# Kernel tuning notes

Measured on AMD Instinct MI355X. Metric: run time of the kernel, lower is better.

The kernel has to match this reference:

```python
import jax, jax.numpy as jnp
import numpy as np

B, S, N_IN, N_OUT = 4, 192, 256, 1

def setup_inputs() -> dict:
    key = jax.random.key(0)
    ks = jax.random.split(key, 7)
    scale = 1.0 / np.sqrt(N_IN)
    return {
        "h_head": jax.random.normal(ks[0], (B, S, N_IN), jnp.float32),
        "h_dep": jax.random.normal(ks[1], (B, S, N_IN), jnp.float32),
        "h_sib": jax.random.normal(ks[2], (B, S, N_IN), jnp.float32),
        "W_tri": jax.random.normal(ks[3], (N_OUT, N_IN, N_IN, N_IN), jnp.float32) * (scale / N_IN),
        "U_hd": jax.random.normal(ks[4], (N_OUT, N_IN, N_IN), jnp.float32) * scale,
        "V_hs": jax.random.normal(ks[5], (N_OUT, N_IN, N_IN), jnp.float32) * scale,
        "Z_ds": jax.random.normal(ks[6], (N_OUT, N_IN, N_IN), jnp.float32) * scale,
        "bias": jnp.zeros((N_OUT,), jnp.float32),
    }

def reference(h_head, h_dep, h_sib, W_tri, U_hd, V_hs, Z_ds, bias):
    # biaffine terms: [b, x, y, o]
    s_hd = jnp.einsum('bhi,oij,bdj->bhdo', h_head, U_hd, h_dep)
    s_hs = jnp.einsum('bhi,oij,bsj->bhso', h_head, V_hs, h_sib)
    s_ds = jnp.einsum('bdi,oij,bsj->bdso', h_dep, Z_ds, h_sib)
    # trilinear term: note j,k of W_tri appear nowhere else, so they are
    # reduced first (w_red[o,i] = sum_{j,k} W_tri[o,i,j,k]) — same math as
    # torch.einsum('bhi,bdi,bsi,oijk->bhdso', ...).
    w_red = jnp.sum(W_tri, axis=(2, 3))  # [o, i]
    s_tri = jnp.einsum('bhi,bdi,bsi,oi->bhdso', h_head, h_dep, h_sib, w_red)
    scores = (s_tri
              + s_hd[:, :, :, None, :]   # unsqueeze sib axis
              + s_hs[:, :, None, :, :]   # unsqueeze dep axis
              + s_ds[:, None, :, :, :]   # unsqueeze head axis
              + bias)
    return scores[..., 0]  # n_out == 1 -> squeeze last dim
```

## Files before the change

kernel.cpp:

```cpp
#include <hip/hip_runtime.h>
#include <stdint.h>

#define NB 4
#define SS 192
#define NI 256

typedef __attribute__((ext_vector_type(8))) short bf16x8;
typedef __attribute__((ext_vector_type(16))) float f32x16;

__device__ __forceinline__ uint16_t f2bf(float f) {
  union { float f; uint32_t u; } v; v.f = f;
  return (uint16_t)((v.u + 0x7FFFu + ((v.u >> 16) & 1u)) >> 16);
}

__device__ __forceinline__ uint4 pack8(const float4 a, const float4 b) {
  uint4 r;
  r.x = (uint32_t)f2bf(a.x) | ((uint32_t)f2bf(a.y) << 16);
  r.y = (uint32_t)f2bf(a.z) | ((uint32_t)f2bf(a.w) << 16);
  r.z = (uint32_t)f2bf(b.x) | ((uint32_t)f2bf(b.y) << 16);
  r.w = (uint32_t)f2bf(b.z) | ((uint32_t)f2bf(b.w) << 16);
  return r;
}

__device__ __forceinline__ uint32_t bfmul2(uint32_t x, uint32_t y) {
  union { float f; uint32_t u; } xa, xb, ya, yb, r0, r1;
  xa.u = x << 16;        ya.u = y << 16;
  xb.u = x & 0xFFFF0000u; yb.u = y & 0xFFFF0000u;
  r0.f = xa.f * ya.f;
  r1.f = xb.f * yb.f;
  uint32_t lo = (r0.u + 0x7FFFu + ((r0.u >> 16) & 1u)) >> 16;
  uint32_t hi = (r1.u + 0x7FFFu + ((r1.u >> 16) & 1u)) >> 16;
  return lo | (hi << 16);
}


__global__ __launch_bounds__(256) void k0(
    const float* __restrict__ W,
    const float* __restrict__ h_head, const float* __restrict__ h_dep, const float* __restrict__ h_sib,
    const float* __restrict__ U, const float* __restrict__ V, const float* __restrict__ Z,
    float* __restrict__ partial,
    uint16_t* __restrict__ HH, uint16_t* __restrict__ HD, uint16_t* __restrict__ HS,
    uint16_t* __restrict__ U16, uint16_t* __restrict__ V16, uint16_t* __restrict__ Z16) {
  __shared__ float red[4];
  const int bi = blockIdx.x, tid = threadIdx.x;
  if (bi < 2048) {
    const float4* pw = (const float4*)(W + (size_t)bi * 8192);
    float4 a = {0.f, 0.f, 0.f, 0.f};
    #pragma unroll
    for (int it = 0; it < 8; ++it) {
      const float4 v = pw[it * 256 + tid];
      a.x += v.x; a.y += v.y; a.z += v.z; a.w += v.w;
    }
    float s = (a.x + a.y) + (a.z + a.w);
    for (int off = 32; off > 0; off >>= 1) s += __shfl_down(s, off, 64);
    if ((tid & 63) == 0) red[tid >> 6] = s;
    __syncthreads();
    if (tid == 0) partial[bi] = red[0] + red[1] + red[2] + red[3];
    return;
  }
  const int rl = tid >> 5, c8 = tid & 31;
  if (bi < 2144) {
    const int g = (bi - 2048) * 8 + rl;
    const int dst = g * 32 + (c8 ^ (g & 15));
    const int srci = g * 64 + c8 * 2;
    { const float4 x = ((const float4*)h_head)[srci], y = ((const float4*)h_head)[srci + 1];
      ((uint4*)HH)[dst] = pack8(x, y); }
    { const float4 x = ((const float4*)h_dep)[srci], y = ((const float4*)h_dep)[srci + 1];
      ((uint4*)HD)[dst] = pack8(x, y); }
    { const float4 x = ((const float4*)h_sib)[srci], y = ((const float4*)h_sib)[srci + 1];
      ((uint4*)HS)[dst] = pack8(x, y); }
  } else {
    const int g = (bi - 2144) * 8 + rl;
    const int dst = g * 32 + (c8 ^ (g & 15));
    const int srci = g * 64 + c8 * 2;
    { const float4 x = ((const float4*)U)[srci], y = ((const float4*)U)[srci + 1];
      ((uint4*)U16)[dst] = pack8(x, y); }
    { const float4 x = ((const float4*)V)[srci], y = ((const float4*)V)[srci + 1];
      ((uint4*)V16)[dst] = pack8(x, y); }
    { const float4 x = ((const float4*)Z)[srci], y = ((const float4*)Z)[srci + 1];
      ((uint4*)Z16)[dst] = pack8(x, y); }
  }
}

__global__ __launch_bounds__(256, 2) void k_s1(
    const uint16_t* __restrict__ HD, const uint16_t* __restrict__ HS,
    const uint16_t* __restrict__ U16, const uint16_t* __restrict__ V16, const uint16_t* __restrict__ Z16,
    uint16_t* __restrict__ dU16, uint16_t* __restrict__ T216, uint16_t* __restrict__ TZ16) {
  __shared__ __align__(16) uint16_t Ah[192 * 128];
  __shared__ __align__(16) uint16_t Bh[128 * 128];
  const int which = blockIdx.x, nt = blockIdx.y, b = blockIdx.z;
  const uint16_t* As = (which == 0) ? HD : HS;
  const uint16_t* Bs = (which == 0) ? U16 : (which == 1) ? V16 : Z16;
  uint16_t* Os = (which == 0) ? dU16 : (which == 1) ? T216 : TZ16;
  const int tid = threadIdx.x, lane = tid & 63, w = tid >> 6;
  const int l31 = lane & 31, l5 = lane >> 5;
  const int N0 = nt * 128;
  f32x16 acc[6] = {};

  #pragma unroll
  for (int kh = 0; kh < 2; ++kh) {
    const int kbase = kh * 128;
    if (kh) __syncthreads();
    #pragma unroll
    for (int i = 0; i < 12; ++i) {
      const int slot = i * 256 + tid;
      const int row = slot >> 4, ck = slot & 15;
      const uint16_t* src = As + (size_t)(b * SS + row) * NI + kbase + ck * 8;
      __builtin_amdgcn_global_load_lds((const __attribute__((address_space(1))) void*)src,
          (__attribute__((address_space(3))) void*)(Ah + (size_t)slot * 8), 16, 0, 0);
    }
    #pragma unroll
    for (int i = 0; i < 8; ++i) {
      const int slot = i * 256 + tid;
      const int row = slot >> 4, ck = slot & 15;
      const uint16_t* src = Bs + (size_t)(N0 + row) * NI + kbase + ck * 8;
      __builtin_amdgcn_global_load_lds((const __attribute__((address_space(1))) void*)src,
          (__attribute__((address_space(3))) void*)(Bh + (size_t)slot * 8), 16, 0, 0);
    }
    __syncthreads();
    const int brow = w * 32 + l31;
    const int bbyte = brow * 256;
    const int bmask = brow & 15;
    #pragma unroll
    for (int ks = 0; ks < 8; ++ks) {
      const int sl = ks * 2 + l5;
      bf16x8 bf = *reinterpret_cast<const bf16x8*>((const char*)Bh + bbyte + ((sl ^ bmask) << 4));
      #pragma unroll
      for (int mt = 0; mt < 6; ++mt) {
        const int ar = mt * 32 + l31;
        bf16x8 af = *reinterpret_cast<const bf16x8*>((const char*)Ah + ar * 256 + ((sl ^ (ar & 15)) << 4));
        acc[mt] = __builtin_amdgcn_mfma_f32_32x32x16_bf16(af, bf, acc[mt], 0, 0, 0);
      }
    }
  }
  const int n = N0 + w * 32 + l31;
  const int nck = n >> 3, npos = n & 7;
  #pragma unroll
  for (int mt = 0; mt < 6; ++mt) {
    #pragma unroll
    for (int r = 0; r < 16; ++r) {
      const int m = mt * 32 + (r & 3) + 8 * (r >> 2) + 4 * l5;
      Os[(size_t)(b * SS + m) * NI + ((nck ^ (m & 15)) << 3) + npos] = f2bf(acc[mt][r]);
    }
  }
}

__global__ __launch_bounds__(384, 1) void k_s2(
    const uint16_t* __restrict__ HH, const uint16_t* __restrict__ HD,
    const uint16_t* __restrict__ dU16, const uint16_t* __restrict__ T216, const uint16_t* __restrict__ TZ16,
    float* __restrict__ s_hd, float* __restrict__ s_hs, float* __restrict__ s_ds) {
  __shared__ __align__(16) uint16_t Ah[192 * 128];
  __shared__ __align__(16) uint16_t Bh[192 * 128];
  const int which = blockIdx.x, b = blockIdx.y;
  const uint16_t* As = (which == 2) ? HD : HH;
  const uint16_t* Bs = (which == 0) ? dU16 : (which == 1) ? T216 : TZ16;
  float* Os = (which == 0) ? s_hd : (which == 1) ? s_hs : s_ds;
  const int tid = threadIdx.x, lane = tid & 63, w = tid >> 6;
  const int l31 = lane & 31, l5 = lane >> 5;
  f32x16 acc[6] = {};

  #pragma unroll
  for (int kh = 0; kh < 2; ++kh) {
    const int kbase = kh * 128;
    if (kh) __syncthreads();
    #pragma unroll
    for (int i = 0; i < 8; ++i) {
      const int slot = i * 384 + tid;
      const int row = slot >> 4, ck = slot & 15;
      const uint16_t* src = As + (size_t)(b * SS + row) * NI + kbase + ck * 8;
      __builtin_amdgcn_global_load_lds((const __attribute__((address_space(1))) void*)src,
          (__attribute__((address_space(3))) void*)(Ah + (size_t)slot * 8), 16, 0, 0);
    }
    #pragma unroll
    for (int i = 0; i < 8; ++i) {
      const int slot = i * 384 + tid;
      const int row = slot >> 4, ck = slot & 15;
      const uint16_t* src = Bs + (size_t)(b * SS + row) * NI + kbase + ck * 8;
      __builtin_amdgcn_global_load_lds((const __attribute__((address_space(1))) void*)src,
          (__attribute__((address_space(3))) void*)(Bh + (size_t)slot * 8), 16, 0, 0);
    }
    __syncthreads();
    const int brow = w * 32 + l31;
    const int bbyte = brow * 256;
    const int bmask = brow & 15;
    #pragma unroll
    for (int ks = 0; ks < 8; ++ks) {
      const int sl = ks * 2 + l5;
      bf16x8 bf = *reinterpret_cast<const bf16x8*>((const char*)Bh + bbyte + ((sl ^ bmask) << 4));
      #pragma unroll
      for (int mt = 0; mt < 6; ++mt) {
        const int ar = mt * 32 + l31;
        bf16x8 af = *reinterpret_cast<const bf16x8*>((const char*)Ah + ar * 256 + ((sl ^ (ar & 15)) << 4));
        acc[mt] = __builtin_amdgcn_mfma_f32_32x32x16_bf16(af, bf, acc[mt], 0, 0, 0);
      }
    }
  }
  const int n = w * 32 + l31;
  #pragma unroll
  for (int mt = 0; mt < 6; ++mt) {
    #pragma unroll
    for (int r = 0; r < 16; ++r) {
      const int m = mt * 32 + (r & 3) + 8 * (r >> 2) + 4 * l5;
      Os[(size_t)(b * SS + m) * SS + n] = acc[mt][r];
    }
  }
}

__global__ __launch_bounds__(576) void k3_big(
    const uint16_t* __restrict__ HH, const uint16_t* __restrict__ HS,
    const float* __restrict__ h_dep, const float* __restrict__ partial,
    const float* __restrict__ s_hd, const float* __restrict__ s_hs,
    const float* __restrict__ s_ds,
    const float* __restrict__ bias, float* __restrict__ out) {
  __shared__ __align__(16) uint16_t Btile[96 * 128];
  __shared__ __align__(16) uint16_t Atile[96 * 128];
  __shared__ uint16_t cvec[NI];
  const int d = blockIdx.x, hb = blockIdx.y >> 1, sb = blockIdx.y & 1, b = blockIdx.z;
  const int tid = threadIdx.x;
  const int lane = tid & 63, w = tid >> 6;
  const int wh = w / 3, ws = w % 3;
  const int l31 = lane & 31, l5 = lane >> 5;

  if (tid < NI) {
    float wr = 0.f;
    #pragma unroll
    for (int q = 0; q < 8; ++q) wr += partial[8 * tid + q];
    cvec[tid] = f2bf(wr * h_dep[(b * SS + d) * NI + tid]);
  }
  __syncthreads();

  f32x16 acc = {};

  #pragma unroll
  for (int half = 0; half < 2; ++half) {
    const int kbase = half * 128;
    if (half) __syncthreads();
    #pragma unroll
    for (int i = 0; i < 3; ++i) {
      const int slot = i * 576 + tid;
      if (slot < 1536) {
        const int row = slot >> 4;
        const uint16_t* src = HS + ((size_t)(b * SS + sb * 96 + row) << 8) + kbase + (slot & 15) * 8;
        __builtin_amdgcn_global_load_lds(
            (const __attribute__((address_space(1))) void*)src,
            (__attribute__((address_space(3))) void*)(Btile + (size_t)slot * 8),
            16, 0, 0);
      }
    }
    #pragma unroll
    for (int i = 0; i < 3; ++i) {
      const int slot = i * 576 + tid;
      if (slot < 1536) {
        const int row = slot >> 4;
        const int kc = slot & 15;
        const int lcl = kc ^ (row & 15);
        const uint4 cv4 = *(const uint4*)(cvec + kbase + lcl * 8);
        const uint4 hh4 = *(const uint4*)(HH + ((size_t)(b * SS + hb * 96 + row) << 8) + kbase + kc * 8);
        uint4 a4;
        a4.x = bfmul2(hh4.x, cv4.x);
        a4.y = bfmul2(hh4.y, cv4.y);
        a4.z = bfmul2(hh4.z, cv4.z);
        a4.w = bfmul2(hh4.w, cv4.w);
        *(uint4*)((char*)Atile + (size_t)slot * 16) = a4;
      }
    }
    __syncthreads();
    const int arow = wh * 32 + l31;
    const int abyte = arow * 256;
    const int amask = arow & 15;
    const int brow = ws * 32 + l31;
    const int bbyte = brow * 256;
    const int bmask = brow & 15;
    #pragma unroll
    for (int ks = 0; ks < 8; ++ks) {
      const int sl = ks * 2 + l5;
      bf16x8 af = *reinterpret_cast<const bf16x8*>((const char*)Atile + abyte + ((sl ^ amask) << 4));
      bf16x8 bf = *reinterpret_cast<const bf16x8*>((const char*)Btile + bbyte + ((sl ^ bmask) << 4));
      acc = __builtin_amdgcn_mfma_f32_32x32x16_bf16(af, bf, acc, 0, 0, 0);
    }
  }

  const float bias0 = bias[0];
  const int s = sb * 96 + ws * 32 + l31;
  const float dsv = s_ds[(b * SS + d) * SS + s];
  #pragma unroll
  for (int r = 0; r < 16; ++r) {
    const int h = hb * 96 + wh * 32 + (r & 3) + 8 * (r >> 2) + 4 * l5;
    const float chd = s_hd[(b * SS + h) * SS + d] + bias0;
    const float v = acc[r] + chd + s_hs[(b * SS + h) * SS + s] + dsv;
    out[((size_t)(b * SS + h) * SS + d) * SS + s] = v;
  }
}

extern "C" void kernel_launch(void* const* d_in, const int* in_sizes, int n_in,
                              void* d_out, int out_size, void* d_ws, size_t ws_size,
                              hipStream_t stream) {
  const float* h_head = (const float*)d_in[0];
  const float* h_dep  = (const float*)d_in[1];
  const float* h_sib  = (const float*)d_in[2];
  const float* W_tri  = (const float*)d_in[3];
  const float* U_hd   = (const float*)d_in[4];
  const float* V_hs   = (const float*)d_in[5];
  const float* Z_ds   = (const float*)d_in[6];
  const float* bias   = (const float*)d_in[7];
  float* out = (float*)d_out;

  float* ws = (float*)d_ws;
  float* partial = ws;          ws += 2048;
  float* s_hd    = ws;          ws += NB * SS * SS;
  float* s_hs    = ws;          ws += NB * SS * SS;
  float* s_ds    = ws;          ws += NB * SS * SS;
  uint16_t* HH   = (uint16_t*)ws;
  uint16_t* HD   = HH + NB * SS * NI;
  uint16_t* HS   = HD + NB * SS * NI;
  uint16_t* U16  = HS + NB * SS * NI;
  uint16_t* V16  = U16 + NI * NI;
  uint16_t* Z16  = V16 + NI * NI;
  uint16_t* dU16 = Z16 + NI * NI;
  uint16_t* T216 = dU16 + NB * SS * NI;
  uint16_t* TZ16 = T216 + NB * SS * NI;

  k0<<<2176, 256, 0, stream>>>(W_tri, h_head, h_dep, h_sib, U_hd, V_hs, Z_ds,
                               partial, HH, HD, HS, U16, V16, Z16);
  k_s1<<<dim3(3, 2, NB), 256, 0, stream>>>(HD, HS, U16, V16, Z16, dU16, T216, TZ16);
  k_s2<<<dim3(3, NB), 384, 0, stream>>>(HH, HD, dU16, T216, TZ16, s_hd, s_hs, s_ds);
  k3_big<<<dim3(SS, 4, NB), 576, 0, stream>>>(HH, HS, h_dep, partial,
                                              s_hd, s_hs, s_ds, bias, out);
}
```

Before: 78.07 us.

## Fold biaffine terms into main MFMA kernel and merge prep kernels

Merges the W reduction, bf16 conversion and first-stage projections into one kernel, converting fp32 inputs inline, and drops the second biaffine GEMM kernel. The big kernel now adds the biaffine terms through extra MFMA passes over K using broadcast vectors and the T2/TZ projections, instead of reading s_hd/s_hs/s_ds. This removes two launches and the intermediate score round trips. In exchange the main kernel does three times more MFMA and staging work per block, with more syncs, and the s_ds/s_hd terms are now rounded through bf16.

```diff
diff --git a/kernel.cpp b/kernel.cpp
--- a/kernel.cpp
+++ b/kernel.cpp
@@ -34,17 +34,19 @@
 }
 
 
-__global__ __launch_bounds__(256) void k0(
+__global__ __launch_bounds__(256) void kA(
     const float* __restrict__ W,
     const float* __restrict__ h_head, const float* __restrict__ h_dep, const float* __restrict__ h_sib,
     const float* __restrict__ U, const float* __restrict__ V, const float* __restrict__ Z,
     float* __restrict__ partial,
-    uint16_t* __restrict__ HH, uint16_t* __restrict__ HD, uint16_t* __restrict__ HS,
-    uint16_t* __restrict__ U16, uint16_t* __restrict__ V16, uint16_t* __restrict__ Z16) {
-  __shared__ float red[4];
+    uint16_t* __restrict__ HH, uint16_t* __restrict__ HS,
+    uint16_t* __restrict__ dU16, uint16_t* __restrict__ T216, uint16_t* __restrict__ TZ16) {
   const int bi = blockIdx.x, tid = threadIdx.x;
-  if (bi < 2048) {
-    const float4* pw = (const float4*)(W + (size_t)bi * 8192);
+
+  if (bi >= 120) {
+    __shared__ float red[4];
+    const int c = bi - 120;
+    const float4* pw = (const float4*)(W + (size_t)c * 8192);
     float4 a = {0.f, 0.f, 0.f, 0.f};
     #pragma unroll
     for (int it = 0; it < 8; ++it) {
@@ -55,166 +57,93 @@
     for (int off = 32; off > 0; off >>= 1) s += __shfl_down(s, off, 64);
     if ((tid & 63) == 0) red[tid >> 6] = s;
     __syncthreads();
-    if (tid == 0) partial[bi] = red[0] + red[1] + red[2] + red[3];
+    if (tid == 0) partial[c] = red[0] + red[1] + red[2] + red[3];
     return;
   }
-  const int rl = tid >> 5, c8 = tid & 31;
-  if (bi < 2144) {
-    const int g = (bi - 2048) * 8 + rl;
+  if (bi >= 24) {
+    const int rl = tid >> 5, c8 = tid & 31;
+    const int g = (bi - 24) * 8 + rl;
     const int dst = g * 32 + (c8 ^ (g & 15));
     const int srci = g * 64 + c8 * 2;
     { const float4 x = ((const float4*)h_head)[srci], y = ((const float4*)h_head)[srci + 1];
       ((uint4*)HH)[dst] = pack8(x, y); }
-    { const float4 x = ((const float4*)h_dep)[srci], y = ((const float4*)h_dep)[srci + 1];
-      ((uint4*)HD)[dst] = pack8(x, y); }
     { const float4 x = ((const float4*)h_sib)[srci], y = ((const float4*)h_sib)[srci + 1];
       ((uint4*)HS)[dst] = pack8(x, y); }
-  } else {
-    const int g = (bi - 2144) * 8 + rl;
-    const int dst = g * 32 + (c8 ^ (g & 15));
-    const int srci = g * 64 + c8 * 2;
-    { const float4 x = ((const float4*)U)[srci], y = ((const float4*)U)[srci + 1];
-      ((uint4*)U16)[dst] = pack8(x, y); }
-    { const float4 x = ((const float4*)V)[srci], y = ((const float4*)V)[srci + 1];
-      ((uint4*)V16)[dst] = pack8(x, y); }
-    { const float4 x = ((const float4*)Z)[srci], y = ((const float4*)Z)[srci + 1];
-      ((uint4*)Z16)[dst] = pack8(x, y); }
-  }
-}
-
-__global__ __launch_bounds__(256, 2) void k_s1(
-    const uint16_t* __restrict__ HD, const uint16_t* __restrict__ HS,
-    const uint16_t* __restrict__ U16, const uint16_t* __restrict__ V16, const uint16_t* __restrict__ Z16,
-    uint16_t* __restrict__ dU16, uint16_t* __restrict__ T216, uint16_t* __restrict__ TZ16) {
-  __shared__ __align__(16) uint16_t Ah[192 * 128];
-  __shared__ __align__(16) uint16_t Bh[128 * 128];
-  const int which = blockIdx.x, nt = blockIdx.y, b = blockIdx.z;
-  const uint16_t* As = (which == 0) ? HD : HS;
-  const uint16_t* Bs = (which == 0) ? U16 : (which == 1) ? V16 : Z16;
-  uint16_t* Os = (which == 0) ? dU16 : (which == 1) ? T216 : TZ16;
-  const int tid = threadIdx.x, lane = tid & 63, w = tid >> 6;
-  const int l31 = lane & 31, l5 = lane >> 5;
-  const int N0 = nt * 128;
-  f32x16 acc[6] = {};
-
-  #pragma unroll
-  for (int kh = 0; kh < 2; ++kh) {
-    const int kbase = kh * 128;
-    if (kh) __syncthreads();
-    #pragma unroll
-    for (int i = 0; i < 12; ++i) {
-      const int slot = i * 256 + tid;
-      const int row = slot >> 4, ck = slot & 15;
-      const uint16_t* src = As + (size_t)(b * SS + row) * NI + kbase + ck * 8;
-      __builtin_amdgcn_global_load_lds((const __attribute__((address_space(1))) void*)src,
-          (__attribute__((address_space(3))) void*)(Ah + (size_t)slot * 8), 16, 0, 0);
-    }
-    #pragma unroll
-    for (int i = 0; i < 8; ++i) {
-      const int slot = i * 256 + tid;
-      const int row = slot >> 4, ck = slot & 15;
-      const uint16_t* src = Bs + (size_t)(N0 + row) * NI + kbase + ck * 8;
-      __builtin_amdgcn_global_load_lds((const __attribute__((address_space(1))) void*)src,
-          (__attribute__((address_space(3))) void*)(Bh + (size_t)slot * 8), 16, 0, 0);
-    }
-    __syncthreads();
-    const int brow = w * 32 + l31;
-    const int bbyte = brow * 256;
-    const int bmask = brow & 15;
-    #pragma unroll
-    for (int ks = 0; ks < 8; ++ks) {
-      const int sl = ks * 2 + l5;
-      bf16x8 bf = *reinterpret_cast<const bf16x8*>((const char*)Bh + bbyte + ((sl ^ bmask) << 4));
-      #pragma unroll
-      for (int mt = 0; mt < 6; ++mt) {
-        const int ar = mt * 32 + l31;
-        bf16x8 af = *reinterpret_cast<const bf16x8*>((const char*)Ah + ar * 256 + ((sl ^ (ar & 15)) << 4));
-        acc[mt] = __builtin_amdgcn_mfma_f32_32x32x16_bf16(af, bf, acc[mt], 0, 0, 0);
-      }
-    }
-  }
-  const int n = N0 + w * 32 + l31;
-  const int nck = n >> 3, npos = n & 7;
-  #pragma unroll
-  for (int mt = 0; mt < 6; ++mt) {
-    #pragma unroll
-    for (int r = 0; r < 16; ++r) {
-      const int m = mt * 32 + (r & 3) + 8 * (r >> 2) + 4 * l5;
-      Os[(size_t)(b * SS + m) * NI + ((nck ^ (m & 15)) << 3) + npos] = f2bf(acc[mt][r]);
-    }
-  }
-}
-
-__global__ __launch_bounds__(384, 1) void k_s2(
-    const uint16_t* __restrict__ HH, const uint16_t* __restrict__ HD,
+    return;
+  }
+
+  {
+    __shared__ __align__(16) uint16_t Ah[192 * 128];
+    __shared__ __align__(16) uint16_t Bh[128 * 128];
+    const int which = bi >> 3, rem = bi & 7;
+    const int b = rem >> 1, nt = rem & 1;
+    const float* As = (which == 0) ? h_dep : h_sib;
+    const float* Bs = (which == 0) ? U : (which == 1) ? V : Z;
+    uint16_t* Os = (which == 0) ? dU16 : (which == 1) ? T216 : TZ16;
+    const int lane = tid & 63, w = tid >> 6;
+    const int l31 = lane & 31, l5 = lane >> 5;
+    const int N0 = nt * 128;
+    f32x16 acc[6] = {};
+
+    #pragma unroll
+    for (int kh = 0; kh < 2; ++kh) {
+      const int kbase = kh * 128;
+      if (kh) __syncthreads();
+      #pragma unroll
+      for (int i = 0; i < 12; ++i) {
+        const int slot = i * 256 + tid;
+        const int row = slot >> 4, ck = slot & 15;
+        const float* sp = As + (size_t)(b * SS + row) * NI + kbase + ck * 8;
+        const float4 x = *(const float4*)sp, y = *(const float4*)(sp + 4);
+        *(uint4*)((char*)Ah + row * 256 + ((ck ^ (row & 15)) << 4)) = pack8(x, y);
+      }
+      #pragma unroll
+      for (int i = 0; i < 8; ++i) {
+        const int slot = i * 256 + tid;
+        const int row = slot >> 4, ck = slot & 15;
+        const float* sp = Bs + (size_t)(N0 + row) * NI + kbase + ck * 8;
+        const float4 x = *(const float4*)sp, y = *(const float4*)(sp + 4);
+        *(uint4*)((char*)Bh + row * 256 + ((ck ^ (row & 15)) << 4)) = pack8(x, y);
+      }
+      __syncthreads();
+      const int brow = w * 32 + l31;
+      const int bbyte = brow * 256;
+      const int bmask = brow & 15;
+      #pragma unroll
+      for (int ks = 0; ks < 8; ++ks) {
+        const int sl = ks * 2 + l5;
+        bf16x8 bf = *reinterpret_cast<const bf16x8*>((const char*)Bh + bbyte + ((sl ^ bmask) << 4));
+        #pragma unroll
+        for (int mt = 0; mt < 6; ++mt) {
+          const int ar = mt * 32 + l31;
+          bf16x8 af = *reinterpret_cast<const bf16x8*>((const char*)Ah + ar * 256 + ((sl ^ (ar & 15)) << 4));
+          acc[mt] = __builtin_amdgcn_mfma_f32_32x32x16_bf16(af, bf, acc[mt], 0, 0, 0);
+        }
+      }
+    }
+    const int n = N0 + w * 32 + l31;
+    const int nck = n >> 3, npos = n & 7;
+    #pragma unroll
+    for (int mt = 0; mt < 6; ++mt) {
+      #pragma unroll
+      for (int r = 0; r < 16; ++r) {
+        const int m = mt * 32 + (r & 3) + 8 * (r >> 2) + 4 * l5;
+        Os[(size_t)(b * SS + m) * NI + ((nck ^ (m & 15)) << 3) + npos] = f2bf(acc[mt][r]);
+      }
+    }
+  }
+}
+
+__global__ __launch_bounds__(576) void kB(
+    const uint16_t* __restrict__ HH, const uint16_t* __restrict__ HS,
     const uint16_t* __restrict__ dU16, const uint16_t* __restrict__ T216, const uint16_t* __restrict__ TZ16,
-    float* __restrict__ s_hd, float* __restrict__ s_hs, float* __restrict__ s_ds) {
-  __shared__ __align__(16) uint16_t Ah[192 * 128];
-  __shared__ __align__(16) uint16_t Bh[192 * 128];
-  const int which = blockIdx.x, b = blockIdx.y;
-  const uint16_t* As = (which == 2) ? HD : HH;
-  const uint16_t* Bs = (which == 0) ? dU16 : (which == 1) ? T216 : TZ16;
-  float* Os = (which == 0) ? s_hd : (which == 1) ? s_hs : s_ds;
-  const int tid = threadIdx.x, lane = tid & 63, w = tid >> 6;
-  const int l31 = lane & 31, l5 = lane >> 5;
-  f32x16 acc[6] = {};
-
-  #pragma unroll
-  for (int kh = 0; kh < 2; ++kh) {
-    const int kbase = kh * 128;
-    if (kh) __syncthreads();
-    #pragma unroll
-    for (int i = 0; i < 8; ++i) {
-      const int slot = i * 384 + tid;
-      const int row = slot >> 4, ck = slot & 15;
-      const uint16_t* src = As + (size_t)(b * SS + row) * NI + kbase + ck * 8;
-      __builtin_amdgcn_global_load_lds((const __attribute__((address_space(1))) void*)src,
-          (__attribute__((address_space(3))) void*)(Ah + (size_t)slot * 8), 16, 0, 0);
-    }
-    #pragma unroll
-    for (int i = 0; i < 8; ++i) {
-      const int slot = i * 384 + tid;
-      const int row = slot >> 4, ck = slot & 15;
-      const uint16_t* src = Bs + (size_t)(b * SS + row) * NI + kbase + ck * 8;
-      __builtin_amdgcn_global_load_lds((const __attribute__((address_space(1))) void*)src,
-          (__attribute__((address_space(3))) void*)(Bh + (size_t)slot * 8), 16, 0, 0);
-    }
-    __syncthreads();
-    const int brow = w * 32 + l31;
-    const int bbyte = brow * 256;
-    const int bmask = brow & 15;
-    #pragma unroll
-    for (int ks = 0; ks < 8; ++ks) {
-      const int sl = ks * 2 + l5;
-      bf16x8 bf = *reinterpret_cast<const bf16x8*>((const char*)Bh + bbyte + ((sl ^ bmask) << 4));
-      #pragma unroll
-      for (int mt = 0; mt < 6; ++mt) {
-        const int ar = mt * 32 + l31;
-        bf16x8 af = *reinterpret_cast<const bf16x8*>((const char*)Ah + ar * 256 + ((sl ^ (ar & 15)) << 4));
-        acc[mt] = __builtin_amdgcn_mfma_f32_32x32x16_bf16(af, bf, acc[mt], 0, 0, 0);
-      }
-    }
-  }
-  const int n = w * 32 + l31;
-  #pragma unroll
-  for (int mt = 0; mt < 6; ++mt) {
-    #pragma unroll
-    for (int r = 0; r < 16; ++r) {
-      const int m = mt * 32 + (r & 3) + 8 * (r >> 2) + 4 * l5;
-      Os[(size_t)(b * SS + m) * SS + n] = acc[mt][r];
-    }
-  }
-}
-
-__global__ __launch_bounds__(576) void k3_big(
-    const uint16_t* __restrict__ HH, const uint16_t* __restrict__ HS,
     const float* __restrict__ h_dep, const float* __restrict__ partial,
-    const float* __restrict__ s_hd, const float* __restrict__ s_hs,
-    const float* __restrict__ s_ds,
     const float* __restrict__ bias, float* __restrict__ out) {
   __shared__ __align__(16) uint16_t Btile[96 * 128];
   __shared__ __align__(16) uint16_t Atile[96 * 128];
-  __shared__ uint16_t cvec[NI];
+  __shared__ __align__(16) uint16_t cvec[NI];
+  __shared__ __align__(16) uint16_t cvec2[NI];
+  __shared__ __align__(16) uint16_t cvec3[NI];
   const int d = blockIdx.x, hb = blockIdx.y >> 1, sb = blockIdx.y & 1, b = blockIdx.z;
   const int tid = threadIdx.x;
   const int lane = tid & 63, w = tid >> 6;
@@ -222,74 +151,115 @@
   const int l31 = lane & 31, l5 = lane >> 5;
 
   if (tid < NI) {
+    const float hd = h_dep[(b * SS + d) * NI + tid];
     float wr = 0.f;
     #pragma unroll
     for (int q = 0; q < 8; ++q) wr += partial[8 * tid + q];
-    cvec[tid] = f2bf(wr * h_dep[(b * SS + d) * NI + tid]);
+    cvec[tid] = f2bf(wr * hd);
+    cvec2[tid] = f2bf(hd);
+  } else if (tid < NI + 32) {
+    const int ck = tid - NI;
+    ((uint4*)cvec3)[ck] = *(const uint4*)(dU16 + (size_t)(b * SS + d) * NI + ((ck ^ (d & 15)) << 3));
   }
   __syncthreads();
 
+  const int arow = wh * 32 + l31, abyte = arow * 256, amask = arow & 15;
+  const int brow = ws * 32 + l31, bbyte = brow * 256, bmask = brow & 15;
   f32x16 acc = {};
 
-  #pragma unroll
-  for (int half = 0; half < 2; ++half) {
-    const int kbase = half * 128;
-    if (half) __syncthreads();
-    #pragma unroll
-    for (int i = 0; i < 3; ++i) {
-      const int slot = i * 576 + tid;
-      if (slot < 1536) {
-        const int row = slot >> 4;
-        const uint16_t* src = HS + ((size_t)(b * SS + sb * 96 + row) << 8) + kbase + (slot & 15) * 8;
-        __builtin_amdgcn_global_load_lds(
-            (const __attribute__((address_space(1))) void*)src,
-            (__attribute__((address_space(3))) void*)(Btile + (size_t)slot * 8),
-            16, 0, 0);
-      }
-    }
-    #pragma unroll
-    for (int i = 0; i < 3; ++i) {
-      const int slot = i * 576 + tid;
-      if (slot < 1536) {
-        const int row = slot >> 4;
-        const int kc = slot & 15;
-        const int lcl = kc ^ (row & 15);
-        const uint4 cv4 = *(const uint4*)(cvec + kbase + lcl * 8);
-        const uint4 hh4 = *(const uint4*)(HH + ((size_t)(b * SS + hb * 96 + row) << 8) + kbase + kc * 8);
-        uint4 a4;
-        a4.x = bfmul2(hh4.x, cv4.x);
-        a4.y = bfmul2(hh4.y, cv4.y);
-        a4.z = bfmul2(hh4.z, cv4.z);
-        a4.w = bfmul2(hh4.w, cv4.w);
-        *(uint4*)((char*)Atile + (size_t)slot * 16) = a4;
-      }
-    }
-    __syncthreads();
-    const int arow = wh * 32 + l31;
-    const int abyte = arow * 256;
-    const int amask = arow & 15;
-    const int brow = ws * 32 + l31;
-    const int bbyte = brow * 256;
-    const int bmask = brow & 15;
-    #pragma unroll
-    for (int ks = 0; ks < 8; ++ks) {
-      const int sl = ks * 2 + l5;
-      bf16x8 af = *reinterpret_cast<const bf16x8*>((const char*)Atile + abyte + ((sl ^ amask) << 4));
-      bf16x8 bf = *reinterpret_cast<const bf16x8*>((const char*)Btile + bbyte + ((sl ^ bmask) << 4));
-      acc = __builtin_amdgcn_mfma_f32_32x32x16_bf16(af, bf, acc, 0, 0, 0);
-    }
-  }
+  #define STAGE_A_MUL(kbase)                                                          \
+    _Pragma("unroll")                                                                 \
+    for (int i = 0; i < 3; ++i) {                                                     \
+      const int slot = i * 576 + tid;                                                 \
+      if (slot < 1536) {                                                              \
+        const int row = slot >> 4, kc = slot & 15;                                    \
+        const int lcl = kc ^ (row & 15);                                              \
+        const uint4 cv4 = *(const uint4*)(cvec + (kbase) + lcl * 8);                  \
+        const uint4 hh4 = *(const uint4*)(HH + ((size_t)(b * SS + hb * 96 + row) << 8) + (kbase) + kc * 8); \
+        uint4 a4;                                                                     \
+        a4.x = bfmul2(hh4.x, cv4.x); a4.y = bfmul2(hh4.y, cv4.y);                     \
+        a4.z = bfmul2(hh4.z, cv4.z); a4.w = bfmul2(hh4.w, cv4.w);                     \
+        *(uint4*)((char*)Atile + (size_t)slot * 16) = a4;                             \
+      }                                                                               \
+    }
+
+  #define STAGE_A_COPY(kbase)                                                         \
+    _Pragma("unroll")                                                                 \
+    for (int i = 0; i < 3; ++i) {                                                     \
+      const int slot = i * 576 + tid;                                                 \
+      if (slot < 1536) {                                                              \
+        const int row = slot >> 4;                                                    \
+        const uint16_t* src = HH + ((size_t)(b * SS + hb * 96 + row) << 8) + (kbase) + (slot & 15) * 8; \
+        __builtin_amdgcn_global_load_lds((const __attribute__((address_space(1))) void*)src, \
+            (__attribute__((address_space(3))) void*)(Atile + (size_t)slot * 8), 16, 0, 0); \
+      }                                                                               \
+    }
+
+  #define STAGE_B(S, kbase)                                                           \
+    _Pragma("unroll")                                                                 \
+    for (int i = 0; i < 3; ++i) {                                                     \
+      const int slot = i * 576 + tid;                                                 \
+      if (slot < 1536) {                                                              \
+        const int row = slot >> 4;                                                    \
+        const uint16_t* src = (S) + ((size_t)(b * SS + sb * 96 + row) << 8) + (kbase) + (slot & 15) * 8; \
+        __builtin_amdgcn_global_load_lds((const __attribute__((address_space(1))) void*)src, \
+            (__attribute__((address_space(3))) void*)(Btile + (size_t)slot * 8), 16, 0, 0); \
+      }                                                                               \
+    }
+
+  #define MM()                                                                        \
+    _Pragma("unroll")                                                                 \
+    for (int ks = 0; ks < 8; ++ks) {                                                  \
+      const int sl = ks * 2 + l5;                                                     \
+      bf16x8 af = *reinterpret_cast<const bf16x8*>((const char*)Atile + abyte + ((sl ^ amask) << 4)); \
+      bf16x8 bf = *reinterpret_cast<const bf16x8*>((const char*)Btile + bbyte + ((sl ^ bmask) << 4)); \
+      acc = __builtin_amdgcn_mfma_f32_32x32x16_bf16(af, bf, acc, 0, 0, 0);            \
+    }
+
+  #define MM_BBCAST(koff)                                                             \
+    _Pragma("unroll")                                                                 \
+    for (int ks = 0; ks < 8; ++ks) {                                                  \
+      const int sl = ks * 2 + l5;                                                     \
+      bf16x8 af = *reinterpret_cast<const bf16x8*>((const char*)Atile + abyte + ((sl ^ amask) << 4)); \
+      bf16x8 bf = *reinterpret_cast<const bf16x8*>(cvec3 + (koff) + sl * 8);          \
+      acc = __builtin_amdgcn_mfma_f32_32x32x16_bf16(af, bf, acc, 0, 0, 0);            \
+    }
+
+  #define MM_ABCAST(koff)                                                             \
+    _Pragma("unroll")                                                                 \
+    for (int ks = 0; ks < 8; ++ks) {                                                  \
+      const int sl = ks * 2 + l5;                                                     \
+      bf16x8 af = *reinterpret_cast<const bf16x8*>(cvec2 + (koff) + sl * 8);          \
+      bf16x8 bf = *reinterpret_cast<const bf16x8*>((const char*)Btile + bbyte + ((sl ^ bmask) << 4)); \
+      acc = __builtin_amdgcn_mfma_f32_32x32x16_bf16(af, bf, acc, 0, 0, 0);            \
+    }
+
+  STAGE_A_MUL(0); STAGE_B(HS, 0); __syncthreads();
+  MM(); __syncthreads();
+  STAGE_A_MUL(128); STAGE_B(HS, 128); __syncthreads();
+  MM(); __syncthreads();
+  STAGE_A_COPY(0); STAGE_B(T216, 0); __syncthreads();
+  MM(); MM_BBCAST(0); __syncthreads();
+  STAGE_A_COPY(128); STAGE_B(T216, 128); __syncthreads();
+  MM(); MM_BBCAST(128); __syncthreads();
+  STAGE_B(TZ16, 0); __syncthreads();
+  MM_ABCAST(0); __syncthreads();
+  STAGE_B(TZ16, 128); __syncthreads();
+  MM_ABCAST(128);
 
   const float bias0 = bias[0];
   const int s = sb * 96 + ws * 32 + l31;
-  const float dsv = s_ds[(b * SS + d) * SS + s];
   #pragma unroll
   for (int r = 0; r < 16; ++r) {
     const int h = hb * 96 + wh * 32 + (r & 3) + 8 * (r >> 2) + 4 * l5;
-    const float chd = s_hd[(b * SS + h) * SS + d] + bias0;
-    const float v = acc[r] + chd + s_hs[(b * SS + h) * SS + s] + dsv;
-    out[((size_t)(b * SS + h) * SS + d) * SS + s] = v;
-  }
+    out[((size_t)(b * SS + h) * SS + d) * SS + s] = acc[r] + bias0;
+  }
+  #undef STAGE_A_MUL
+  #undef STAGE_A_COPY
+  #undef STAGE_B
+  #undef MM
+  #undef MM_BBCAST
+  #undef MM_ABCAST
 }
 
 extern "C" void kernel_launch(void* const* d_in, const int* in_sizes, int n_in,
@@ -307,23 +277,14 @@
 
   float* ws = (float*)d_ws;
   float* partial = ws;          ws += 2048;
-  float* s_hd    = ws;          ws += NB * SS * SS;
-  float* s_hs    = ws;          ws += NB * SS * SS;
-  float* s_ds    = ws;          ws += NB * SS * SS;
   uint16_t* HH   = (uint16_t*)ws;
-  uint16_t* HD   = HH + NB * SS * NI;
-  uint16_t* HS   = HD + NB * SS * NI;
-  uint16_t* U16  = HS + NB * SS * NI;
-  uint16_t* V16  = U16 + NI * NI;
-  uint16_t* Z16  = V16 + NI * NI;
-  uint16_t* dU16 = Z16 + NI * NI;
+  uint16_t* HS   = HH + NB * SS * NI;
+  uint16_t* dU16 = HS + NB * SS * NI;
   uint16_t* T216 = dU16 + NB * SS * NI;
   uint16_t* TZ16 = T216 + NB * SS * NI;
 
-  k0<<<2176, 256, 0, stream>>>(W_tri, h_head, h_dep, h_sib, U_hd, V_hs, Z_ds,
-                               partial, HH, HD, HS, U16, V16, Z16);
-  k_s1<<<dim3(3, 2, NB), 256, 0, stream>>>(HD, HS, U16, V16, Z16, dU16, T216, TZ16);
-  k_s2<<<dim3(3, NB), 384, 0, stream>>>(HH, HD, dU16, T216, TZ16, s_hd, s_hs, s_ds);
-  k3_big<<<dim3(SS, 4, NB), 576, 0, stream>>>(HH, HS, h_dep, partial,
-                                              s_hd, s_hs, s_ds, bias, out);
-}
+  kA<<<2168, 256, 0, stream>>>(W_tri, h_head, h_dep, h_sib, U_hd, V_hs, Z_ds,
+                               partial, HH, HS, dU16, T216, TZ16);
+  kB<<<dim3(SS, 4, NB), 576, 0, stream>>>(HH, HS, dU16, T216, TZ16,
+                                          h_dep, partial, bias, out);
+}
```

Result: slower. 118.6 us (+52.0%).

## Fuse first-stage biaffine GEMM into the conversion/W-reduction kernel

Applied to the files above, without the earlier changes.

Merges the k_s1 GEMM into the first kernel, scheduling its 24 GEMM blocks first in the grid so they run alongside the W_tri reduction and activation conversion blocks. The GEMM blocks now read fp32 h_dep/h_sib and U/V/Z directly and convert to bf16 while staging into swizzled LDS, which removes the separate U/V/Z conversion pass, its workspace buffers, and one kernel launch boundary. In exchange the fused kernel carries the large LDS footprint for every block, which may reduce occupancy of the many reduction blocks. The GEMM blocks also load fp32 data synchronously instead of using async global-to-LDS copies.

```diff
diff --git a/kernel.cpp b/kernel.cpp
--- a/kernel.cpp
+++ b/kernel.cpp
@@ -34,17 +34,19 @@
 }
 
 
-__global__ __launch_bounds__(256) void k0(
+__global__ __launch_bounds__(256) void kA(
     const float* __restrict__ W,
     const float* __restrict__ h_head, const float* __restrict__ h_dep, const float* __restrict__ h_sib,
     const float* __restrict__ U, const float* __restrict__ V, const float* __restrict__ Z,
     float* __restrict__ partial,
     uint16_t* __restrict__ HH, uint16_t* __restrict__ HD, uint16_t* __restrict__ HS,
-    uint16_t* __restrict__ U16, uint16_t* __restrict__ V16, uint16_t* __restrict__ Z16) {
-  __shared__ float red[4];
+    uint16_t* __restrict__ dU16, uint16_t* __restrict__ T216, uint16_t* __restrict__ TZ16) {
   const int bi = blockIdx.x, tid = threadIdx.x;
-  if (bi < 2048) {
-    const float4* pw = (const float4*)(W + (size_t)bi * 8192);
+
+  if (bi >= 120) {
+    __shared__ float red[4];
+    const int c = bi - 120;
+    const float4* pw = (const float4*)(W + (size_t)c * 8192);
     float4 a = {0.f, 0.f, 0.f, 0.f};
     #pragma unroll
     for (int it = 0; it < 8; ++it) {
@@ -55,12 +57,12 @@
     for (int off = 32; off > 0; off >>= 1) s += __shfl_down(s, off, 64);
     if ((tid & 63) == 0) red[tid >> 6] = s;
     __syncthreads();
-    if (tid == 0) partial[bi] = red[0] + red[1] + red[2] + red[3];
+    if (tid == 0) partial[c] = red[0] + red[1] + red[2] + red[3];
     return;
   }
-  const int rl = tid >> 5, c8 = tid & 31;
-  if (bi < 2144) {
-    const int g = (bi - 2048) * 8 + rl;
+  if (bi >= 24) {
+    const int rl = tid >> 5, c8 = tid & 31;
+    const int g = (bi - 24) * 8 + rl;
     const int dst = g * 32 + (c8 ^ (g & 15));
     const int srci = g * 64 + c8 * 2;
     { const float4 x = ((const float4*)h_head)[srci], y = ((const float4*)h_head)[srci + 1];
@@ -69,78 +71,67 @@
       ((uint4*)HD)[dst] = pack8(x, y); }
     { const float4 x = ((const float4*)h_sib)[srci], y = ((const float4*)h_sib)[srci + 1];
       ((uint4*)HS)[dst] = pack8(x, y); }
-  } else {
-    const int g = (bi - 2144) * 8 + rl;
-    const int dst = g * 32 + (c8 ^ (g & 15));
-    const int srci = g * 64 + c8 * 2;
-    { const float4 x = ((const float4*)U)[srci], y = ((const float4*)U)[srci + 1];
-      ((uint4*)U16)[dst] = pack8(x, y); }
-    { const float4 x = ((const float4*)V)[srci], y = ((const float4*)V)[srci + 1];
-      ((uint4*)V16)[dst] = pack8(x, y); }
-    { const float4 x = ((const float4*)Z)[srci], y = ((const float4*)Z)[srci + 1];
-      ((uint4*)Z16)[dst] = pack8(x, y); }
-  }
-}
-
-__global__ __launch_bounds__(256, 2) void k_s1(
-    const uint16_t* __restrict__ HD, const uint16_t* __restrict__ HS,
-    const uint16_t* __restrict__ U16, const uint16_t* __restrict__ V16, const uint16_t* __restrict__ Z16,
-    uint16_t* __restrict__ dU16, uint16_t* __restrict__ T216, uint16_t* __restrict__ TZ16) {
-  __shared__ __align__(16) uint16_t Ah[192 * 128];
-  __shared__ __align__(16) uint16_t Bh[128 * 128];
-  const int which = blockIdx.x, nt = blockIdx.y, b = blockIdx.z;
-  const uint16_t* As = (which == 0) ? HD : HS;
-  const uint16_t* Bs = (which == 0) ? U16 : (which == 1) ? V16 : Z16;
-  uint16_t* Os = (which == 0) ? dU16 : (which == 1) ? T216 : TZ16;
-  const int tid = threadIdx.x, lane = tid & 63, w = tid >> 6;
-  const int l31 = lane & 31, l5 = lane >> 5;
-  const int N0 = nt * 128;
-  f32x16 acc[6] = {};
-
-  #pragma unroll
-  for (int kh = 0; kh < 2; ++kh) {
-    const int kbase = kh * 128;
-    if (kh) __syncthreads();
-    #pragma unroll
-    for (int i = 0; i < 12; ++i) {
-      const int slot = i * 256 + tid;
-      const int row = slot >> 4, ck = slot & 15;
-      const uint16_t* src = As + (size_t)(b * SS + row) * NI + kbase + ck * 8;
-      __builtin_amdgcn_global_load_lds((const __attribute__((address_space(1))) void*)src,
-          (__attribute__((address_space(3))) void*)(Ah + (size_t)slot * 8), 16, 0, 0);
-    }
-    #pragma unroll
-    for (int i = 0; i < 8; ++i) {
-      const int slot = i * 256 + tid;
-      const int row = slot >> 4, ck = slot & 15;
-      const uint16_t* src = Bs + (size_t)(N0 + row) * NI + kbase + ck * 8;
-      __builtin_amdgcn_global_load_lds((const __attribute__((address_space(1))) void*)src,
-          (__attribute__((address_space(3))) void*)(Bh + (size_t)slot * 8), 16, 0, 0);
-    }
-    __syncthreads();
-    const int brow = w * 32 + l31;
-    const int bbyte = brow * 256;
-    const int bmask = brow & 15;
-    #pragma unroll
-    for (int ks = 0; ks < 8; ++ks) {
-      const int sl = ks * 2 + l5;
-      bf16x8 bf = *reinterpret_cast<const bf16x8*>((const char*)Bh + bbyte + ((sl ^ bmask) << 4));
-      #pragma unroll
-      for (int mt = 0; mt < 6; ++mt) {
-        const int ar = mt * 32 + l31;
-        bf16x8 af = *reinterpret_cast<const bf16x8*>((const char*)Ah + ar * 256 + ((sl ^ (ar & 15)) << 4));
-        acc[mt] = __builtin_amdgcn_mfma_f32_32x32x16_bf16(af, bf, acc[mt], 0, 0, 0);
-      }
-    }
-  }
-  const int n = N0 + w * 32 + l31;
-  const int nck = n >> 3, npos = n & 7;
-  #pragma unroll
-  for (int mt = 0; mt < 6; ++mt) {
-    #pragma unroll
-    for (int r = 0; r < 16; ++r) {
-      const int m = mt * 32 + (r & 3) + 8 * (r >> 2) + 4 * l5;
-      Os[(size_t)(b * SS + m) * NI + ((nck ^ (m & 15)) << 3) + npos] = f2bf(acc[mt][r]);
+    return;
+  }
+
+  {
+    __shared__ __align__(16) uint16_t Ah[192 * 128];
+    __shared__ __align__(16) uint16_t Bh[128 * 128];
+    const int which = bi >> 3, rem = bi & 7;
+    const int b = rem >> 1, nt = rem & 1;
+    const float* As = (which == 0) ? h_dep : h_sib;
+    const float* Bs = (which == 0) ? U : (which == 1) ? V : Z;
+    uint16_t* Os = (which == 0) ? dU16 : (which == 1) ? T216 : TZ16;
+    const int lane = tid & 63, w = tid >> 6;
+    const int l31 = lane & 31, l5 = lane >> 5;
+    const int N0 = nt * 128;
+    f32x16 acc[6] = {};
+
+    #pragma unroll
+    for (int kh = 0; kh < 2; ++kh) {
+      const int kbase = kh * 128;
+      if (kh) __syncthreads();
+      #pragma unroll
+      for (int i = 0; i < 12; ++i) {
+        const int slot = i * 256 + tid;
+        const int row = slot >> 4, ck = slot & 15;
+        const float* sp = As + (size_t)(b * SS + row) * NI + kbase + ck * 8;
+        const float4 x = *(const float4*)sp, y = *(const float4*)(sp + 4);
+        *(uint4*)((char*)Ah + row * 256 + ((ck ^ (row & 15)) << 4)) = pack8(x, y);
+      }
+      #pragma unroll
+      for (int i = 0; i < 8; ++i) {
+        const int slot = i * 256 + tid;
+        const int row = slot >> 4, ck = slot & 15;
+        const float* sp = Bs + (size_t)(N0 + row) * NI + kbase + ck * 8;
+        const float4 x = *(const float4*)sp, y = *(const float4*)(sp + 4);
+        *(uint4*)((char*)Bh + row * 256 + ((ck ^ (row & 15)) << 4)) = pack8(x, y);
+      }
+      __syncthreads();
+      const int brow = w * 32 + l31;
+      const int bbyte = brow * 256;
+      const int bmask = brow & 15;
+      #pragma unroll
+      for (int ks = 0; ks < 8; ++ks) {
+        const int sl = ks * 2 + l5;
+        bf16x8 bf = *reinterpret_cast<const bf16x8*>((const char*)Bh + bbyte + ((sl ^ bmask) << 4));
+        #pragma unroll
+        for (int mt = 0; mt < 6; ++mt) {
+          const int ar = mt * 32 + l31;
+          bf16x8 af = *reinterpret_cast<const bf16x8*>((const char*)Ah + ar * 256 + ((sl ^ (ar & 15)) << 4));
+          acc[mt] = __builtin_amdgcn_mfma_f32_32x32x16_bf16(af, bf, acc[mt], 0, 0, 0);
+        }
+      }
+    }
+    const int n = N0 + w * 32 + l31;
+    const int nck = n >> 3, npos = n & 7;
+    #pragma unroll
+    for (int mt = 0; mt < 6; ++mt) {
+      #pragma unroll
+      for (int r = 0; r < 16; ++r) {
+        const int m = mt * 32 + (r & 3) + 8 * (r >> 2) + 4 * l5;
+        Os[(size_t)(b * SS + m) * NI + ((nck ^ (m & 15)) << 3) + npos] = f2bf(acc[mt][r]);
+      }
     }
   }
 }
@@ -313,16 +304,12 @@
   uint16_t* HH   = (uint16_t*)ws;
   uint16_t* HD   = HH + NB * SS * NI;
   uint16_t* HS   = HD + NB * SS * NI;
-  uint16_t* U16  = HS + NB * SS * NI;
-  uint16_t* V16  = U16 + NI * NI;
-  uint16_t* Z16  = V16 + NI * NI;
-  uint16_t* dU16 = Z16 + NI * NI;
+  uint16_t* dU16 = HS + NB * SS * NI;
   uint16_t* T216 = dU16 + NB * SS * NI;
   uint16_t* TZ16 = T216 + NB * SS * NI;
 
-  k0<<<2176, 256, 0, stream>>>(W_tri, h_head, h_dep, h_sib, U_hd, V_hs, Z_ds,
-                               partial, HH, HD, HS, U16, V16, Z16);
-  k_s1<<<dim3(3, 2, NB), 256, 0, stream>>>(HD, HS, U16, V16, Z16, dU16, T216, TZ16);
+  kA<<<2168, 256, 0, stream>>>(W_tri, h_head, h_dep, h_sib, U_hd, V_hs, Z_ds,
+                               partial, HH, HD, HS, dU16, T216, TZ16);
   k_s2<<<dim3(3, NB), 384, 0, stream>>>(HH, HD, dU16, T216, TZ16, s_hd, s_hs, s_ds);
   k3_big<<<dim3(SS, 4, NB), 576, 0, stream>>>(HH, HS, h_dep, partial,
                                               s_hd, s_hs, s_ds, bias, out);
```

After: 73.60 us. 5.7% less time.
